# Kernel tuning notes

Hardware: AMD Instinct MI355X
Metric: run time of the kernel (lower is better)

The kernel has to match this reference:

```python
import jax, jax.numpy as jnp
import numpy as np

B, N, DIM, H, DH = 1, 2048, 1024, 16, 64


def setup_inputs() -> dict:
    key = jax.random.key(0)
    k1, k2, k3 = jax.random.split(key, 3)
    x = jax.random.normal(k1, (B, N, DIM), dtype=jnp.float32)
    # LinearNoBias(dim, 6*heads*dim_head): weight [6*H*DH, DIM]
    w_qkv = jax.random.normal(k2, (6 * H * DH, DIM), dtype=jnp.float32) * (DIM ** -0.5)
    # LinearNoBias(heads*dim_head, dim): weight [DIM, H*DH]
    w_out = jax.random.normal(k3, (DIM, H * DH), dtype=jnp.float32) * ((H * DH) ** -0.5)
    return {"x": x, "w_qkv": w_qkv, "w_out": w_out}


def reference(x, w_qkv, w_out):
    b, n, _ = x.shape
    scale = DH ** -0.5
    qkvs = x @ w_qkv.T  # [b, n, 6*H*DH]
    # rearrange 'b n (qkv h d) -> qkv b h n d'
    qkvs = qkvs.reshape(b, n, 6, H, DH).transpose(2, 0, 3, 1, 4)
    qu, ku, vu, qc, kc, vc = qkvs
    qu = qu * scale
    qc = qc * scale

    upper = jnp.triu(jnp.ones((n, n), dtype=bool), 1)  # strict upper triangle

    # term1: causal (lower-incl-diag) qc . vu
    term1 = jnp.einsum('bhid,bhjd->bhij', qc, vu)
    term1 = jnp.where(upper, 0.0, term1)

    # sigmoid lookahead term: strict-upper only
    sig = jax.nn.sigmoid(jnp.einsum('bhid,bhjd->bhij', qu, ku))
    sig = jnp.where(upper, sig, 0.0)

    Su = jnp.einsum('bhij,bhkj->bhik', term1, sig)

    Sc = jnp.einsum('bhid,bhjd->bhij', qc, kc)
    neg = -jnp.finfo(Sc.dtype).max
    Sc = jnp.where(upper, neg, Sc)

    scores = Sc - jax.nn.silu(Su)
    attn = jax.nn.softmax(scores, axis=-1)
    out = jnp.einsum('bhij,bhjd->bhid', attn, vc)  # [b,h,n,d]
    out = out.transpose(0, 2, 1, 3).reshape(b, n, H * DH)
    return out @ w_out.T
```

## Files before the change

kernel.cpp:

```cpp
#include <hip/hip_runtime.h>

using f16 = _Float16;
using half8  = __attribute__((ext_vector_type(8))) f16;
using half4v = __attribute__((ext_vector_type(4))) f16;
using float4v = __attribute__((ext_vector_type(4))) float;

#define DEV static __device__ __forceinline__

constexpr int N = 2048, DIM = 1024, H = 16, DH = 64, F6 = 6144;
constexpr int LDSH = 136;
constexpr int TS = 128 * 128;
constexpr int NTILES = 136;
constexpr int KD = 2048 * 64;


DEV int PL(int i, int k) { return i * (i + 1) / 2 + k; }
DEV int PU(int a, int b) { return a * 16 - a * (a - 1) / 2 + (b - a); }

template<int ROWS, int THREADS>
DEV void stage64(const f16* __restrict__ g, int strideHalves, f16* lds, int tid) {
#pragma unroll
  for (int q = 0; q < (ROWS * 8) / THREADS; ++q) {
    const int chunk = q * THREADS + tid;
    const int m = chunk >> 3, c = (chunk & 7) ^ (m & 7);
    const f16* gp = g + (size_t)m * strideHalves + c * 8;
    __builtin_amdgcn_global_load_lds(
        (const __attribute__((address_space(1))) unsigned int*)gp,
        (__attribute__((address_space(3))) unsigned int*)(lds + chunk * 8), 16, 0, 0);
  }
}

template<int ELEMS, int THREADS>
DEV void stage_panel(const f16* __restrict__ g, f16* lds, int tid) {
#pragma unroll
  for (int i = 0; i < ELEMS / 8 / THREADS; ++i) {
    const int chunk = i * THREADS + tid;
    __builtin_amdgcn_global_load_lds(
        (const __attribute__((address_space(1))) unsigned int*)(g + (size_t)chunk * 8),
        (__attribute__((address_space(3))) unsigned int*)(lds + chunk * 8), 16, 0, 0);
  }
}

DEV half8 rdfrag(const f16* T, int m, int ks, int q) {
  const int c = (ks * 4 + q) ^ (m & 7);
  return *(const half8*)(T + m * 64 + c * 8);
}

DEV void wfrag(f16* T, int row, int col, f16 v) {
  T[row * 64 + ((((col >> 3) ^ (row & 7)) << 3) | (col & 7))] = v;
}

DEV void gemm64(const f16* As, const f16* Bs, int wm, int wn, int l, float4v acc[4][4]) {
  const int q = l >> 4, mm = l & 15;
#pragma unroll
  for (int ks = 0; ks < 2; ++ks) {
    half8 af[4], bf[4];
#pragma unroll
    for (int mi = 0; mi < 4; ++mi) af[mi] = rdfrag(As, wm + mm + mi * 16, ks, q);
#pragma unroll
    for (int ni = 0; ni < 4; ++ni) bf[ni] = rdfrag(Bs, wn + mm + ni * 16, ks, q);
#pragma unroll
    for (int mi = 0; mi < 4; ++mi)
#pragma unroll
      for (int ni = 0; ni < 4; ++ni)
        acc[mi][ni] = __builtin_amdgcn_mfma_f32_16x16x32_f16(af[mi], bf[ni], acc[mi][ni], 0, 0, 0);
  }
}

DEV void decode_pair(int p, int& ti, int& tk) {
  int t = (int)((sqrtf(8.f * p + 1.f) - 1.f) * 0.5f);
  while (t * (t + 1) / 2 > p) --t;
  while ((t + 1) * (t + 2) / 2 <= p) ++t;
  const int i2 = p - t * (t + 1) / 2;
  ti = (15 - t) + i2;
  tk = i2;
}

__global__ __launch_bounds__(256) void k_cast(const float* __restrict__ s, f16* __restrict__ d, int n4) {
  int i = blockIdx.x * 256 + threadIdx.x;
  if (i < n4) {
    float4 v = ((const float4*)s)[i];
    half4v h;
    h[0] = (f16)v.x; h[1] = (f16)v.y; h[2] = (f16)v.z; h[3] = (f16)v.w;
    ((half4v*)d)[i] = h;
  }
}

__global__ __launch_bounds__(256) void k_qkv(const f16* __restrict__ xh, const f16* __restrict__ wh,
                                             f16* __restrict__ quh, f16* __restrict__ kuh,
                                             f16* __restrict__ vuh, f16* __restrict__ qch,
                                             f16* __restrict__ kch, f16* __restrict__ vcT,
                                             f16* __restrict__ vuT) {
  __shared__ __align__(16) f16 lds[128 * LDSH];
  f16* As = lds; f16* Bs = lds + 128 * 64;
  const int tid = threadIdx.x, w = tid >> 6, l = tid & 63;
  const int tm = blockIdx.x * 128, tf = blockIdx.y * 128;
  const int wm = (w >> 1) * 64, wn = (w & 1) * 64;
  float4v acc[4][4] = {};
  for (int k0 = 0; k0 < DIM; k0 += 64) {
    stage64<128, 256>(xh + (size_t)tm * DIM + k0, DIM, As, tid);
    stage64<128, 256>(wh + (size_t)tf * DIM + k0, DIM, Bs, tid);
    __syncthreads();
    gemm64(As, Bs, wm, wn, l, acc);
    __syncthreads();
  }
  const int rbase = (l >> 4) * 4, cidx = l & 15;
  const int t = tf >> 10;
  const float sc = (t == 0 || t == 3) ? 0.125f : 1.f;
  if (t == 5 || t == 2) {
#pragma unroll
    for (int mi = 0; mi < 4; ++mi)
#pragma unroll
      for (int ni = 0; ni < 4; ++ni) {
        const int f = tf + wn + ni * 16 + cidx;
        const int h = (f & 1023) >> 6, d = f & 63;
        const int n = tm + wm + mi * 16 + rbase;
        half4v p;
#pragma unroll
        for (int r = 0; r < 4; ++r) p[r] = (f16)acc[mi][ni][r];
        if (t == 5) {
          const int ks2 = (n & 63) >> 5, q2 = (n >> 3) & 3;
          const int inner = ks2 * 256 + q2 * 64 + (d >> 4) * 16 + (d & 15);
          *(half4v*)(vcT + (size_t)h * DH * N + (size_t)(n >> 6) * 4096 +
                     (size_t)inner * 8 + (n & 7)) = p;
        } else {
          *(half4v*)(vuT + ((size_t)h * DH + d) * N + n) = p;
        }
      }
  }
  if (t != 5) {
#pragma unroll
    for (int mi = 0; mi < 4; ++mi)
#pragma unroll
      for (int ni = 0; ni < 4; ++ni)
#pragma unroll
        for (int r = 0; r < 4; ++r)
          lds[(wm + mi * 16 + rbase + r) * LDSH + wn + ni * 16 + cidx] = (f16)(acc[mi][ni][r] * sc);
    __syncthreads();
    const int hb = (tf & 1023) >> 6;
    if (t == 4) {
#pragma unroll
      for (int qq = 0; qq < 8; ++qq) {
        const int idx = qq * 256 + tid;
        const int hh = idx >> 10, f = idx & 1023;
        const int pl = f >> 9, inner = f & 511;
        const int m2 = inner & 15, ni2 = (inner >> 4) & 3, q2 = (inner >> 6) & 3, ks2 = inner >> 8;
        const int row = pl * 64 + ni2 * 16 + m2;
        const int col = hh * 64 + ks2 * 32 + q2 * 8;
        *(half8*)(kch + (size_t)(hb + hh) * N * DH + ((size_t)(tm >> 6) + pl) * 4096 +
                  (size_t)inner * 8) = *(const half8*)(lds + row * LDSH + col);
      }
    } else {
      f16* dst = (t == 0) ? quh : (t == 1) ? kuh : (t == 2) ? vuh : qch;
#pragma unroll
      for (int q = 0; q < 8; ++q) {
        const int idx = q * 256 + tid, row = idx >> 4, c = idx & 15;
        const int h = hb + (c >> 3), d0 = (c & 7) * 8, n = tm + row;
        *(half8*)(dst + ((size_t)h * N + n) * DH + d0) = *(const half8*)(lds + row * LDSH + c * 8);
      }
    }
  }
}

__global__ __launch_bounds__(256) void k_dsig(const f16* __restrict__ quh, const f16* __restrict__ kuh,
                                              const f16* __restrict__ qch, const f16* __restrict__ vuh,
                                              const f16* __restrict__ vuT,
                                              f16* __restrict__ sigb, f16* __restrict__ DC,
                                              f16* __restrict__ diagb, int h0) {
  __shared__ __align__(16) f16 L[32768];
  f16* quA = L; f16* kuB = L + 8192; f16* s1 = L + 16384; f16* s2 = L + 24576;
  int b, a;
  decode_pair(blockIdx.y, b, a);
  const int hl = blockIdx.x, h = h0 + hl;
  const int tid = threadIdx.x, w = tid >> 6, l = tid & 63;
  const int q = l >> 4, m = l & 15;
  const int wm = (w >> 1) * 64, wn = (w & 1) * 64;
  const size_t ho = (size_t)h * N * DH;

  stage64<128, 256>(quh + ho + (size_t)(a * 128) * DH, DH, quA, tid);
  stage64<128, 256>(kuh + ho + (size_t)(b * 128) * DH, DH, kuB, tid);
  __syncthreads();
  float4v acc[4][4] = {};
  gemm64(quA, kuB, wm, wn, l, acc);
  __syncthreads();
  stage64<64, 256>(vuT + (size_t)h * DH * N + b * 128, N, kuB, tid);
  stage64<64, 256>(vuT + (size_t)h * DH * N + b * 128 + 64, N, kuB + 4096, tid);
#pragma unroll
  for (int mi = 0; mi < 4; ++mi)
#pragma unroll
    for (int ni = 0; ni < 4; ++ni)
#pragma unroll
      for (int r = 0; r < 4; ++r) {
        const int row = wm + mi * 16 + q * 4 + r;
        const int col = wn + ni * 16 + m;
        const float x = acc[mi][ni][r];
        const f16 sv = (b * 128 + col > a * 128 + row) ? (f16)(1.f / (1.f + __expf(-x))) : (f16)0.f;
        wfrag((col < 64) ? s1 : s2, row, col & 63, sv);
      }
  __syncthreads();
  {
    f16* Sg = sigb + ((size_t)hl * NTILES + PU(a, b)) * TS;
#pragma unroll
    for (int qq = 0; qq < 8; ++qq) {
      const int idx = qq * 256 + tid;
      const int hf = idx >> 10, inner = idx & 1023;
      const int m2 = inner & 15, ni2 = (inner >> 4) & 3, q2 = (inner >> 6) & 3, ks2 = inner >> 8;
      const int row = hf * 64 + ni2 * 16 + m2;
      const int c8 = ks2 * 4 + q2;
      const f16* p = ((c8 >> 3) ? s2 : s1) + row * 64 + (((c8 & 7) ^ (row & 7)) << 3);
      *(half8*)(Sg + (size_t)idx * 8) = *(const half8*)p;
    }
  }
  float4v dacc[2][4] = {};
#pragma unroll
  for (int p = 0; p < 2; ++p)
#pragma unroll
    for (int ks = 0; ks < 2; ++ks) {
      half8 bf[4], af[2];
#pragma unroll
      for (int ni = 0; ni < 4; ++ni) bf[ni] = rdfrag(kuB + p * 4096, ni * 16 + m, ks, q);
#pragma unroll
      for (int mi = 0; mi < 2; ++mi) af[mi] = rdfrag(p ? s2 : s1, w * 32 + mi * 16 + m, ks, q);
#pragma unroll
      for (int mi = 0; mi < 2; ++mi)
#pragma unroll
        for (int ni = 0; ni < 4; ++ni)
          dacc[mi][ni] = __builtin_amdgcn_mfma_f32_16x16x32_f16(af[mi], bf[ni], dacc[mi][ni], 0, 0, 0);
    }
  __syncthreads();
  if (a == b) {
    stage64<128, 256>(qch + ho + (size_t)(a * 128) * DH, DH, quA, tid);
    stage64<128, 256>(vuh + ho + (size_t)(a * 128) * DH, DH, kuB, tid);
  }
  {
    f16* epsD = s1;
#pragma unroll
    for (int mi = 0; mi < 2; ++mi)
#pragma unroll
      for (int ni = 0; ni < 4; ++ni)
#pragma unroll
        for (int r = 0; r < 4; ++r)
          epsD[(w * 32 + mi * 16 + q * 4 + r) * 68 + ni * 16 + m] = (f16)dacc[mi][ni][r];
    __syncthreads();
    f16* Dg = DC + ((size_t)hl * 16 + b) * KD + (size_t)a * 8192;
#pragma unroll
    for (int qq = 0; qq < 4; ++qq) {
      const int idx = qq * 256 + tid;
      const int pl = idx >> 9, inner = idx & 511;
      const int m2 = inner & 15, ni2 = (inner >> 4) & 3, q2 = (inner >> 6) & 3, ks2 = inner >> 8;
      const int row = pl * 64 + ni2 * 16 + m2;
      const int c = ks2 * 4 + q2;
      *(half8*)(Dg + (size_t)idx * 8) = *(const half8*)(epsD + row * 68 + c * 8);
    }
  }
  if (a == b) {
    float4v tacc[4][4] = {};
    gemm64(quA, kuB, wm, wn, l, tacc);
    f16* Tg = diagb + ((size_t)hl * 16 + a) * TS;
#pragma unroll
    for (int mi = 0; mi < 4; ++mi)
#pragma unroll
      for (int ni = 0; ni < 4; ++ni)
#pragma unroll
        for (int r = 0; r < 4; ++r) {
          const int row = wm + mi * 16 + q * 4 + r, col = wn + ni * 16 + m;
          Tg[(size_t)row * 128 + col] = (col <= row) ? (f16)tacc[mi][ni][r] : (f16)0.f;
        }
  }
}

__global__ __launch_bounds__(256) void k_scan(f16* __restrict__ DC, int total) {
  const int idx = blockIdx.x * 256 + threadIdx.x;
  if (idx >= total) return;
  const int g = idx >> 17, off = idx & (KD - 1);
  const int a = off >> 13;
  f16* p = DC + (size_t)g * 16 * KD + off;
  float s = 0.f;
#pragma unroll
  for (int T = 0; T < 16; ++T) {
    const float v = (T >= a) ? (float)p[(size_t)T * KD] : 0.f;
    p[(size_t)T * KD] = (f16)s;
    s += v;
  }
}

__global__ __launch_bounds__(128) void k_favs(const f16* __restrict__ qch, const f16* __restrict__ kch,
                                              const f16* __restrict__ DC, const f16* __restrict__ sigb,
                                              const f16* __restrict__ diagb, const f16* __restrict__ vcT,
                                              f16* __restrict__ Oh, int h0) {
  __shared__ __align__(16) f16 L[2 * 12288 + 2 * 1024];
  const int hl = blockIdx.x, h = h0 + hl;
  const int mt = 63 - (int)blockIdx.y;
  const int tid = threadIdx.x, w = tid >> 6, l = tid & 63;
  const int q = l >> 4, m = l & 15;
  const int ti = mt >> 2, r0 = mt * 32;
  const size_t ho = (size_t)h * N * DH;
  const f16* qc = qch + ho;
  const f16* kcb = kch + ho;
  const f16* Cb = DC + ((size_t)hl * 16 + ti) * KD;
  const f16* Td = diagb + ((size_t)hl * 16 + ti) * TS;
  const f16* Sgb = sigb + (size_t)hl * NTILES * TS;
  const f16* V = vcT + (size_t)h * DH * N;
  f16* pw = L + 24576 + w * 1024;
  const int lo = q * 512 + m * 8;

  const int rr = w * 16 + m;
  half8 qcA[2], tdA[4];
  const int dr = (mt & 3) * 32 + rr;
#pragma unroll
  for (int ks = 0; ks < 2; ++ks)
    qcA[ks] = *(const half8*)(qc + (size_t)(r0 + rr) * DH + ks * 32 + q * 8);
#pragma unroll
  for (int ks = 0; ks < 4; ++ks)
    tdA[ks] = *(const half8*)(Td + (size_t)dr * 128 + ks * 32 + q * 8);

  float4v o[4] = {};
  float mrun[4], lrun[4];
#pragma unroll
  for (int r = 0; r < 4; ++r) { mrun[r] = -1e30f; lrun[r] = 0.f; }

  const int jtmax = mt >> 1;
  stage_panel<4096, 128>(Cb, L, tid);
  stage_panel<8192, 128>(Sgb + (size_t)PU(0, ti) * TS, L + 4096, tid);

  for (int jt = 0; jt <= jtmax; ++jt) {
    if (jt < jtmax) {
      const int j2 = jt + 1;
      f16* Nb = L + (j2 & 1) * 12288;
      stage_panel<4096, 128>(Cb + (size_t)j2 * 4096, Nb, tid);
      stage_panel<8192, 128>(Sgb + (size_t)PU(j2 >> 1, ti) * TS + (size_t)(j2 & 1) * 8192, Nb + 4096, tid);
      asm volatile("s_waitcnt vmcnt(12)" ::: "memory");
    } else {
      asm volatile("s_waitcnt vmcnt(0)" ::: "memory");
    }
    __builtin_amdgcn_s_barrier();
    __builtin_amdgcn_sched_barrier(0);

    const f16* Bp = L + (jt & 1) * 12288 + lo;
    const f16* Kp = kcb + (size_t)jt * 4096 + lo;
    const f16* Vp = V + (size_t)jt * 4096 + lo;
    half8 bK[2][4];
#pragma unroll
    for (int ks = 0; ks < 2; ++ks)
#pragma unroll
      for (int ni = 0; ni < 4; ++ni) bK[ks][ni] = *(const half8*)(Kp + ks * 2048 + ni * 128);
    float4v s[4] = {};
#pragma unroll
    for (int ks = 0; ks < 2; ++ks) {
      half8 bf[4];
#pragma unroll
      for (int ni = 0; ni < 4; ++ni) bf[ni] = *(const half8*)(Bp + ks * 2048 + ni * 128);
#pragma unroll
      for (int ni = 0; ni < 4; ++ni)
        s[ni] = __builtin_amdgcn_mfma_f32_16x16x32_f16(qcA[ks], bf[ni], s[ni], 0, 0, 0);
    }
#pragma unroll
    for (int ks = 0; ks < 4; ++ks) {
      half8 bf[4];
#pragma unroll
      for (int ni = 0; ni < 4; ++ni) bf[ni] = *(const half8*)(Bp + 4096 + ks * 2048 + ni * 128);
#pragma unroll
      for (int ni = 0; ni < 4; ++ni)
        s[ni] = __builtin_amdgcn_mfma_f32_16x16x32_f16(tdA[ks], bf[ni], s[ni], 0, 0, 0);
    }
    half8 bV[2][4];
#pragma unroll
    for (int ks = 0; ks < 2; ++ks)
#pragma unroll
      for (int ni = 0; ni < 4; ++ni) bV[ks][ni] = *(const half8*)(Vp + ks * 2048 + ni * 128);
#pragma unroll
    for (int ni = 0; ni < 4; ++ni)
#pragma unroll
      for (int r = 0; r < 4; ++r) {
        const float x = s[ni][r];
        s[ni][r] = -(x / (1.f + __expf(-x)));
      }
#pragma unroll
    for (int ks = 0; ks < 2; ++ks)
#pragma unroll
      for (int ni = 0; ni < 4; ++ni)
        s[ni] = __builtin_amdgcn_mfma_f32_16x16x32_f16(qcA[ks], bK[ks][ni], s[ni], 0, 0, 0);
    if (jt == jtmax) {
      const int k0 = jt * 64;
#pragma unroll
      for (int ni = 0; ni < 4; ++ni) {
        const int col = k0 + ni * 16 + m;
#pragma unroll
        for (int r = 0; r < 4; ++r) {
          const int gr = r0 + w * 16 + q * 4 + r;
          if (col > gr) s[ni][r] = -1e30f;
        }
      }
    }
    float al[4], ts[4];
#pragma unroll
    for (int r = 0; r < 4; ++r) {
      float tmx = fmaxf(fmaxf(s[0][r], s[1][r]), fmaxf(s[2][r], s[3][r]));
#pragma unroll
      for (int x = 1; x < 16; x <<= 1) tmx = fmaxf(tmx, __shfl_xor(tmx, x));
      const float nm = fmaxf(mrun[r], tmx);
      al[r] = __expf(mrun[r] - nm);
      mrun[r] = nm;
      ts[r] = 0.f;
    }
#pragma unroll
    for (int ni = 0; ni < 4; ++ni)
#pragma unroll
      for (int r = 0; r < 4; ++r) {
        const float p = __expf(s[ni][r] - mrun[r]);
        wfrag(pw, q * 4 + r, ni * 16 + m, (f16)p);
        ts[r] += p;
      }
#pragma unroll
    for (int r = 0; r < 4; ++r) {
#pragma unroll
      for (int x = 1; x < 16; x <<= 1) ts[r] += __shfl_xor(ts[r], x);
      lrun[r] = lrun[r] * al[r] + ts[r];
#pragma unroll
      for (int ni = 0; ni < 4; ++ni) o[ni][r] *= al[r];
    }
#pragma unroll
    for (int ks = 0; ks < 2; ++ks) {
      half8 af = rdfrag(pw, m, ks, q);
#pragma unroll
      for (int ni = 0; ni < 4; ++ni)
        o[ni] = __builtin_amdgcn_mfma_f32_16x16x32_f16(af, bV[ks][ni], o[ni], 0, 0, 0);
    }
    __builtin_amdgcn_sched_barrier(0);
    __builtin_amdgcn_s_barrier();
  }
#pragma unroll
  for (int r = 0; r < 4; ++r) {
    const float inv = 1.f / lrun[r];
    const int gr = r0 + w * 16 + q * 4 + r;
#pragma unroll
    for (int ni = 0; ni < 4; ++ni)
      Oh[(size_t)gr * (H * DH) + h * DH + ni * 16 + m] = (f16)(o[ni][r] * inv);
  }
}

__global__ __launch_bounds__(256) void k_out(const f16* __restrict__ Oh, const f16* __restrict__ wo,
                                             float* __restrict__ out) {
  __shared__ __align__(16) f16 lds[128 * LDSH];
  f16* As = lds; f16* Bs = lds + 128 * 64;
  const int tid = threadIdx.x, w = tid >> 6, l = tid & 63;
  const int tm = blockIdx.x * 128, tn = blockIdx.y * 128;
  const int wm = (w >> 1) * 64, wn = (w & 1) * 64;
  float4v acc[4][4] = {};
  for (int k0 = 0; k0 < DIM; k0 += 64) {
    stage64<128, 256>(Oh + (size_t)tm * DIM + k0, DIM, As, tid);
    stage64<128, 256>(wo + (size_t)tn * DIM + k0, DIM, Bs, tid);
    __syncthreads();
    gemm64(As, Bs, wm, wn, l, acc);
    __syncthreads();
  }
  const int rbase = (l >> 4) * 4, cidx = l & 15;
#pragma unroll
  for (int mi = 0; mi < 4; ++mi)
#pragma unroll
    for (int ni = 0; ni < 4; ++ni)
#pragma unroll
      for (int r = 0; r < 4; ++r) {
        const int n = tm + wm + mi * 16 + rbase + r;
        const int dmo = tn + wn + ni * 16 + cidx;
        out[(size_t)n * DIM + dmo] = acc[mi][ni][r];
      }
}

extern "C" void kernel_launch(void* const* d_in, const int* in_sizes, int n_in,
                              void* d_out, int out_size, void* d_ws, size_t ws_size,
                              hipStream_t stream) {
  const float* x = (const float*)d_in[0];
  const float* wqkv = (const float*)d_in[1];
  const float* wout = (const float*)d_in[2];
  float* out = (float*)d_out;
  char* ws = (char*)d_ws;

  size_t off = 0;
  auto alloc = [&](size_t b) { size_t o = off; off += (b + 255) & ~(size_t)255; return o; };
  f16* xh  = (f16*)(ws + alloc((size_t)N * DIM * 2));
  f16* wqh = (f16*)(ws + alloc((size_t)F6 * DIM * 2));
  f16* woh = (f16*)(ws + alloc((size_t)DIM * H * DH * 2));
  f16* quh = (f16*)(ws + alloc((size_t)H * N * DH * 2));
  f16* kuh = (f16*)(ws + alloc((size_t)H * N * DH * 2));
  f16* vuh = (f16*)(ws + alloc((size_t)H * N * DH * 2));
  f16* qch = (f16*)(ws + alloc((size_t)H * N * DH * 2));
  f16* kch = (f16*)(ws + alloc((size_t)H * N * DH * 2));
  f16* vcT = (f16*)(ws + alloc((size_t)H * DH * N * 2));
  f16* vuT = (f16*)(ws + alloc((size_t)H * DH * N * 2));
  f16* Oh  = (f16*)(ws + alloc((size_t)N * H * DH * 2));
  const size_t persist = off;

  const size_t per_head = ((size_t)NTILES * TS + (size_t)16 * KD + (size_t)16 * TS) * 2;
  int G = (ws_size > persist + 4096) ? (int)((ws_size - persist - 4096) / per_head) : 1;
  if (G < 1) G = 1;
  if (G > 16) G = 16;
  {
    const int R = (H + G - 1) / G;
    G = (H + R - 1) / R;
  }
  f16* sigb  = (f16*)(ws + alloc((size_t)G * NTILES * TS * 2));
  f16* DC    = (f16*)(ws + alloc((size_t)G * 16 * KD * 2));
  f16* diagb = (f16*)(ws + alloc((size_t)G * 16 * TS * 2));

  k_cast<<<(N * DIM / 4 + 255) / 256, 256, 0, stream>>>(x, xh, N * DIM / 4);
  k_cast<<<(F6 * DIM / 4 + 255) / 256, 256, 0, stream>>>(wqkv, wqh, F6 * DIM / 4);
  k_cast<<<(DIM * H * DH / 4 + 255) / 256, 256, 0, stream>>>(wout, woh, DIM * H * DH / 4);

  k_qkv<<<dim3(N / 128, F6 / 128), 256, 0, stream>>>(xh, wqh, quh, kuh, vuh, qch, kch, vcT, vuT);

  for (int h0 = 0; h0 < H; h0 += G) {
    const int Gr = (H - h0 < G) ? (H - h0) : G;
    k_dsig<<<dim3(Gr, 136), 256, 0, stream>>>(quh, kuh, qch, vuh, vuT, sigb, DC, diagb, h0);
    k_scan<<<(Gr * KD + 255) / 256, 256, 0, stream>>>(DC, Gr * KD);
    k_favs<<<dim3(Gr, 64), 128, 0, stream>>>(qch, kch, DC, sigb, diagb, vcT, Oh, h0);
  }

  k_out<<<dim3(16, 8), 256, 0, stream>>>(Oh, woh, out);
}
```

Measured before the change: 294.8 us.

## Split k_favs key tiles across two wave pairs and merge softmax states

Doubles the k_favs block to 256 threads. Two wave pairs process alternating 64-column key tiles, so each loop iteration covers two tiles, and the pairs combine their online-softmax partials (max, sum, output) through LDS at the end. The DC panel is now read directly from global memory instead of being staged in LDS, and a full 128-column sigmoid tile is staged per iteration. This aims to halve the serial loop length and add parallelism, at the cost of more LDS, a final merge step, and idle waves on odd tile counts.

```diff
diff --git a/kernel.cpp b/kernel.cpp
--- a/kernel.cpp
+++ b/kernel.cpp
@@ -284,15 +284,17 @@
   }
 }
 
-__global__ __launch_bounds__(128) void k_favs(const f16* __restrict__ qch, const f16* __restrict__ kch,
+__global__ __launch_bounds__(256) void k_favs(const f16* __restrict__ qch, const f16* __restrict__ kch,
                                               const f16* __restrict__ DC, const f16* __restrict__ sigb,
                                               const f16* __restrict__ diagb, const f16* __restrict__ vcT,
                                               f16* __restrict__ Oh, int h0) {
-  __shared__ __align__(16) f16 L[2 * 12288 + 2 * 1024];
+  __shared__ __align__(16) f16 L[2 * 16384 + 4 * 1024];
   const int hl = blockIdx.x, h = h0 + hl;
   const int mt = 63 - (int)blockIdx.y;
   const int tid = threadIdx.x, w = tid >> 6, l = tid & 63;
   const int q = l >> 4, m = l & 15;
+  const int d = w >> 1;
+  const int rw = w & 1;
   const int ti = mt >> 2, r0 = mt * 32;
   const size_t ho = (size_t)h * N * DH;
   const f16* qc = qch + ho;
@@ -301,10 +303,10 @@
   const f16* Td = diagb + ((size_t)hl * 16 + ti) * TS;
   const f16* Sgb = sigb + (size_t)hl * NTILES * TS;
   const f16* V = vcT + (size_t)h * DH * N;
-  f16* pw = L + 24576 + w * 1024;
+  f16* pw = L + 32768 + w * 1024;
   const int lo = q * 512 + m * 8;
 
-  const int rr = w * 16 + m;
+  const int rr = rw * 16 + m;
   half8 qcA[2], tdA[4];
   const int dr = (mt & 3) * 32 + rr;
 #pragma unroll
@@ -320,122 +322,149 @@
   for (int r = 0; r < 4; ++r) { mrun[r] = -1e30f; lrun[r] = 0.f; }
 
   const int jtmax = mt >> 1;
-  stage_panel<4096, 128>(Cb, L, tid);
-  stage_panel<8192, 128>(Sgb + (size_t)PU(0, ti) * TS, L + 4096, tid);
-
-  for (int jt = 0; jt <= jtmax; ++jt) {
-    if (jt < jtmax) {
-      const int j2 = jt + 1;
-      f16* Nb = L + (j2 & 1) * 12288;
-      stage_panel<4096, 128>(Cb + (size_t)j2 * 4096, Nb, tid);
-      stage_panel<8192, 128>(Sgb + (size_t)PU(j2 >> 1, ti) * TS + (size_t)(j2 & 1) * 8192, Nb + 4096, tid);
-      asm volatile("s_waitcnt vmcnt(12)" ::: "memory");
+  const int np = jtmax / 2 + 1;
+  stage_panel<16384, 256>(Sgb + (size_t)PU(0, ti) * TS, L, tid);
+
+  for (int p = 0; p < np; ++p) {
+    if (2 * (p + 1) <= jtmax) {
+      stage_panel<16384, 256>(Sgb + (size_t)PU(p + 1, ti) * TS,
+                              L + ((p + 1) & 1) * 16384, tid);
+      asm volatile("s_waitcnt vmcnt(8)" ::: "memory");
     } else {
       asm volatile("s_waitcnt vmcnt(0)" ::: "memory");
     }
     __builtin_amdgcn_s_barrier();
     __builtin_amdgcn_sched_barrier(0);
 
-    const f16* Bp = L + (jt & 1) * 12288 + lo;
-    const f16* Kp = kcb + (size_t)jt * 4096 + lo;
-    const f16* Vp = V + (size_t)jt * 4096 + lo;
-    half8 bK[2][4];
-#pragma unroll
-    for (int ks = 0; ks < 2; ++ks)
-#pragma unroll
-      for (int ni = 0; ni < 4; ++ni) bK[ks][ni] = *(const half8*)(Kp + ks * 2048 + ni * 128);
-    float4v s[4] = {};
-#pragma unroll
-    for (int ks = 0; ks < 2; ++ks) {
-      half8 bf[4];
-#pragma unroll
-      for (int ni = 0; ni < 4; ++ni) bf[ni] = *(const half8*)(Bp + ks * 2048 + ni * 128);
+    const int c = 2 * p + d;
+    if (c <= jtmax) {
+      const f16* Sp = L + (p & 1) * 16384 + d * 8192 + lo;
+      const f16* Cp = Cb + (size_t)c * 4096 + lo;
+      const f16* Kp = kcb + (size_t)c * 4096 + lo;
+      const f16* Vp = V + (size_t)c * 4096 + lo;
+      half8 bC[2][4], bK[2][4];
+#pragma unroll
+      for (int ks = 0; ks < 2; ++ks)
+#pragma unroll
+        for (int ni = 0; ni < 4; ++ni) {
+          bC[ks][ni] = *(const half8*)(Cp + ks * 2048 + ni * 128);
+          bK[ks][ni] = *(const half8*)(Kp + ks * 2048 + ni * 128);
+        }
+      float4v s[4] = {};
+#pragma unroll
+      for (int ks = 0; ks < 2; ++ks)
+#pragma unroll
+        for (int ni = 0; ni < 4; ++ni)
+          s[ni] = __builtin_amdgcn_mfma_f32_16x16x32_f16(qcA[ks], bC[ks][ni], s[ni], 0, 0, 0);
+#pragma unroll
+      for (int ks = 0; ks < 4; ++ks) {
+        half8 bf[4];
+#pragma unroll
+        for (int ni = 0; ni < 4; ++ni) bf[ni] = *(const half8*)(Sp + ks * 2048 + ni * 128);
+#pragma unroll
+        for (int ni = 0; ni < 4; ++ni)
+          s[ni] = __builtin_amdgcn_mfma_f32_16x16x32_f16(tdA[ks], bf[ni], s[ni], 0, 0, 0);
+      }
+      half8 bV[2][4];
+#pragma unroll
+      for (int ks = 0; ks < 2; ++ks)
+#pragma unroll
+        for (int ni = 0; ni < 4; ++ni) bV[ks][ni] = *(const half8*)(Vp + ks * 2048 + ni * 128);
 #pragma unroll
       for (int ni = 0; ni < 4; ++ni)
-        s[ni] = __builtin_amdgcn_mfma_f32_16x16x32_f16(qcA[ks], bf[ni], s[ni], 0, 0, 0);
-    }
-#pragma unroll
-    for (int ks = 0; ks < 4; ++ks) {
-      half8 bf[4];
-#pragma unroll
-      for (int ni = 0; ni < 4; ++ni) bf[ni] = *(const half8*)(Bp + 4096 + ks * 2048 + ni * 128);
+#pragma unroll
+        for (int r = 0; r < 4; ++r) {
+          const float x = s[ni][r];
+          s[ni][r] = -(x / (1.f + __expf(-x)));
+        }
+#pragma unroll
+      for (int ks = 0; ks < 2; ++ks)
+#pragma unroll
+        for (int ni = 0; ni < 4; ++ni)
+          s[ni] = __builtin_amdgcn_mfma_f32_16x16x32_f16(qcA[ks], bK[ks][ni], s[ni], 0, 0, 0);
+      if (c == jtmax) {
+        const int k0 = c * 64;
+#pragma unroll
+        for (int ni = 0; ni < 4; ++ni) {
+          const int col = k0 + ni * 16 + m;
+#pragma unroll
+          for (int r = 0; r < 4; ++r) {
+            const int gr = r0 + rw * 16 + q * 4 + r;
+            if (col > gr) s[ni][r] = -1e30f;
+          }
+        }
+      }
+      float al[4], ts[4];
+#pragma unroll
+      for (int r = 0; r < 4; ++r) {
+        float tmx = fmaxf(fmaxf(s[0][r], s[1][r]), fmaxf(s[2][r], s[3][r]));
+#pragma unroll
+        for (int x = 1; x < 16; x <<= 1) tmx = fmaxf(tmx, __shfl_xor(tmx, x));
+        const float nm = fmaxf(mrun[r], tmx);
+        al[r] = __expf(mrun[r] - nm);
+        mrun[r] = nm;
+        ts[r] = 0.f;
+      }
 #pragma unroll
       for (int ni = 0; ni < 4; ++ni)
-        s[ni] = __builtin_amdgcn_mfma_f32_16x16x32_f16(tdA[ks], bf[ni], s[ni], 0, 0, 0);
-    }
-    half8 bV[2][4];
-#pragma unroll
-    for (int ks = 0; ks < 2; ++ks)
-#pragma unroll
-      for (int ni = 0; ni < 4; ++ni) bV[ks][ni] = *(const half8*)(Vp + ks * 2048 + ni * 128);
-#pragma unroll
-    for (int ni = 0; ni < 4; ++ni)
+#pragma unroll
+        for (int r = 0; r < 4; ++r) {
+          const float pp = __expf(s[ni][r] - mrun[r]);
+          wfrag(pw, q * 4 + r, ni * 16 + m, (f16)pp);
+          ts[r] += pp;
+        }
 #pragma unroll
       for (int r = 0; r < 4; ++r) {
-        const float x = s[ni][r];
-        s[ni][r] = -(x / (1.f + __expf(-x)));
-      }
-#pragma unroll
-    for (int ks = 0; ks < 2; ++ks)
-#pragma unroll
-      for (int ni = 0; ni < 4; ++ni)
-        s[ni] = __builtin_amdgcn_mfma_f32_16x16x32_f16(qcA[ks], bK[ks][ni], s[ni], 0, 0, 0);
-    if (jt == jtmax) {
-      const int k0 = jt * 64;
-#pragma unroll
-      for (int ni = 0; ni < 4; ++ni) {
-        const int col = k0 + ni * 16 + m;
-#pragma unroll
-        for (int r = 0; r < 4; ++r) {
-          const int gr = r0 + w * 16 + q * 4 + r;
-          if (col > gr) s[ni][r] = -1e30f;
-        }
-      }
-    }
-    float al[4], ts[4];
-#pragma unroll
-    for (int r = 0; r < 4; ++r) {
-      float tmx = fmaxf(fmaxf(s[0][r], s[1][r]), fmaxf(s[2][r], s[3][r]));
-#pragma unroll
-      for (int x = 1; x < 16; x <<= 1) tmx = fmaxf(tmx, __shfl_xor(tmx, x));
-      const float nm = fmaxf(mrun[r], tmx);
-      al[r] = __expf(mrun[r] - nm);
-      mrun[r] = nm;
-      ts[r] = 0.f;
-    }
-#pragma unroll
-    for (int ni = 0; ni < 4; ++ni)
-#pragma unroll
-      for (int r = 0; r < 4; ++r) {
-        const float p = __expf(s[ni][r] - mrun[r]);
-        wfrag(pw, q * 4 + r, ni * 16 + m, (f16)p);
-        ts[r] += p;
-      }
-#pragma unroll
-    for (int r = 0; r < 4; ++r) {
-#pragma unroll
-      for (int x = 1; x < 16; x <<= 1) ts[r] += __shfl_xor(ts[r], x);
-      lrun[r] = lrun[r] * al[r] + ts[r];
-#pragma unroll
-      for (int ni = 0; ni < 4; ++ni) o[ni][r] *= al[r];
-    }
-#pragma unroll
-    for (int ks = 0; ks < 2; ++ks) {
-      half8 af = rdfrag(pw, m, ks, q);
-#pragma unroll
-      for (int ni = 0; ni < 4; ++ni)
-        o[ni] = __builtin_amdgcn_mfma_f32_16x16x32_f16(af, bV[ks][ni], o[ni], 0, 0, 0);
+#pragma unroll
+        for (int x = 1; x < 16; x <<= 1) ts[r] += __shfl_xor(ts[r], x);
+        lrun[r] = lrun[r] * al[r] + ts[r];
+#pragma unroll
+        for (int ni = 0; ni < 4; ++ni) o[ni][r] *= al[r];
+      }
+#pragma unroll
+      for (int ks = 0; ks < 2; ++ks) {
+        half8 af = rdfrag(pw, m, ks, q);
+#pragma unroll
+        for (int ni = 0; ni < 4; ++ni)
+          o[ni] = __builtin_amdgcn_mfma_f32_16x16x32_f16(af, bV[ks][ni], o[ni], 0, 0, 0);
+      }
     }
     __builtin_amdgcn_sched_barrier(0);
     __builtin_amdgcn_s_barrier();
   }
-#pragma unroll
-  for (int r = 0; r < 4; ++r) {
-    const float inv = 1.f / lrun[r];
-    const int gr = r0 + w * 16 + q * 4 + r;
+
+  float* OB = (float*)L;
+  float* MB = (float*)L + 2 * 16 * 68;
+  float* LB = MB + 2 * 16;
+  if (d == 1) {
 #pragma unroll
     for (int ni = 0; ni < 4; ++ni)
-      Oh[(size_t)gr * (H * DH) + h * DH + ni * 16 + m] = (f16)(o[ni][r] * inv);
+#pragma unroll
+      for (int r = 0; r < 4; ++r)
+        OB[(rw * 16 + q * 4 + r) * 68 + ni * 16 + m] = o[ni][r];
+    if (m == 0)
+#pragma unroll
+      for (int r = 0; r < 4; ++r) {
+        MB[rw * 16 + q * 4 + r] = mrun[r];
+        LB[rw * 16 + q * 4 + r] = lrun[r];
+      }
+  }
+  __syncthreads();
+  if (d == 0) {
+#pragma unroll
+    for (int r = 0; r < 4; ++r) {
+      const int row = q * 4 + r;
+      const float m2 = MB[rw * 16 + row], l2 = LB[rw * 16 + row];
+      const float ms = fmaxf(mrun[r], m2);
+      const float e1 = __expf(mrun[r] - ms), e2 = __expf(m2 - ms);
+      const float inv = 1.f / (lrun[r] * e1 + l2 * e2);
+      const int gr = r0 + rw * 16 + row;
+#pragma unroll
+      for (int ni = 0; ni < 4; ++ni) {
+        const float ov = o[ni][r] * e1 + OB[(rw * 16 + row) * 68 + ni * 16 + m] * e2;
+        Oh[(size_t)gr * (H * DH) + h * DH + ni * 16 + m] = (f16)(ov * inv);
+      }
+    }
   }
 }
 
@@ -513,7 +542,7 @@
     const int Gr = (H - h0 < G) ? (H - h0) : G;
     k_dsig<<<dim3(Gr, 136), 256, 0, stream>>>(quh, kuh, qch, vuh, vuT, sigb, DC, diagb, h0);
     k_scan<<<(Gr * KD + 255) / 256, 256, 0, stream>>>(DC, Gr * KD);
-    k_favs<<<dim3(Gr, 64), 128, 0, stream>>>(qch, kch, DC, sigb, diagb, vcT, Oh, h0);
+    k_favs<<<dim3(Gr, 64), 256, 0, stream>>>(qch, kch, DC, sigb, diagb, vcT, Oh, h0);
   }
 
   k_out<<<dim3(16, 8), 256, 0, stream>>>(Oh, woh, out);
```

Result: faster. 284.4 us (-3.5%).
